# Kernel optimization log

Measured on AMD Instinct MI355X. Metric: run time of the kernel, lower is better.

## Reference

```python
import jax, jax.numpy as jnp
import numpy as np

N_NODES = 100000
N_EDGES = 1600000
IN_DIM = 256
HID = 64
OUT_DIM = 1
N_GRAPHS = 100


def setup_inputs() -> dict:
    key = jax.random.key(0)
    ks = jax.random.split(key, 12)
    x = jax.random.normal(ks[0], (N_NODES, IN_DIM), dtype=jnp.float32)
    edge_index = jax.random.randint(ks[1], (2, N_EDGES), 0, N_NODES, dtype=jnp.int64 if jax.config.read('jax_enable_x64') else jnp.int32)
    batch = jnp.sort(jax.random.randint(ks[2], (N_NODES,), 0, N_GRAPHS, dtype=jnp.int32))
    def lin(k, fan_in, fan_out):
        bound = 1.0 / np.sqrt(fan_in)
        kw, kb = jax.random.split(k)
        W = jax.random.uniform(kw, (fan_in, fan_out), minval=-bound, maxval=bound, dtype=jnp.float32)
        b = jax.random.uniform(kb, (fan_out,), minval=-bound, maxval=bound, dtype=jnp.float32)
        return W, b
    W1, b1 = lin(ks[3], IN_DIM, HID)
    W2, b2 = lin(ks[4], HID, HID)
    W3, b3 = lin(ks[5], HID, HID)
    Wl, bl = lin(ks[6], HID, OUT_DIM)
    return {"x": x, "edge_index": edge_index, "batch": batch,
            "W1": W1, "b1": b1, "W2": W2, "b2": b2, "W3": W3, "b3": b3,
            "Wl": Wl, "bl": bl}


def _gcn_layer(h, src, dst, norm, W, b):
    # PyG GCNConv: h' = scatter_add(norm * (h @ W)[src] -> dst) + b
    h = h @ W                                   # [N, F_out]
    msg = h[src] * norm[:, None]                # [E+N, F_out] irregular gather
    agg = jax.ops.segment_sum(msg, dst, num_segments=N_NODES)
    return agg + b


def reference(x, edge_index, batch, W1, b1, W2, b2, W3, b3, Wl, bl):
    # add self loops (static shape) as GCNConv does by default
    loops = jnp.arange(N_NODES, dtype=edge_index.dtype)
    src = jnp.concatenate([edge_index[0], loops])  # [E+N]
    dst = jnp.concatenate([edge_index[1], loops])  # [E+N]
    # symmetric normalization: deg over targets incl. self loops
    deg = jax.ops.segment_sum(jnp.ones_like(dst, dtype=x.dtype), dst, num_segments=N_NODES)
    dinv = jnp.where(deg > 0, jax.lax.rsqrt(deg), 0.0)
    norm = dinv[src] * dinv[dst]                # [E+N]

    h = jax.nn.relu(_gcn_layer(x, src, dst, norm, W1, b1))
    h = jax.nn.relu(_gcn_layer(h, src, dst, norm, W2, b2))
    h = _gcn_layer(h, src, dst, norm, W3, b3)   # last conv: no relu

    # global_add_pool over graphs; dropout is identity at inference
    pooled = jax.ops.segment_sum(h, batch, num_segments=N_GRAPHS)  # [G, HID]
    return pooled @ Wl + bl                     # [G, 1]
```

## Files before the change

kernel.cpp:

```cpp
#include <hip/hip_runtime.h>

#define N_NODES 100000
#define N_EDGES 1600000
#define IN_DIM 256
#define HID 64
#define N_GRAPHS 100
#define BSHIFT 8
#define NBUCK 391
#define CHUNK 4096
#define BCAP 5120

typedef __attribute__((ext_vector_type(8))) short short8;
typedef __attribute__((ext_vector_type(8))) unsigned short us8;
typedef __attribute__((ext_vector_type(4))) float floatx4;

__device__ __forceinline__ unsigned short f2b(float f) {
    unsigned int u = __float_as_uint(f);
    unsigned int r = (u + 0x7FFFu + ((u >> 16) & 1u)) >> 16;
    return (unsigned short)r;
}
__device__ __forceinline__ float b2f(unsigned short b) {
    return __uint_as_float(((unsigned int)b) << 16);
}


__global__ void k_prep(const float* __restrict__ W1, const float* __restrict__ W2,
                       const float* __restrict__ W3, const float* __restrict__ Wl,
                       const float* __restrict__ b3,
                       unsigned short* __restrict__ wt1, unsigned short* __restrict__ wt2,
                       float* __restrict__ w3l,
                       int* __restrict__ bcnt, float* __restrict__ partial) {
    int i = blockIdx.x * 256 + threadIdx.x;
    if (i < IN_DIM * HID) {
        int k = i >> 6, n = i & 63;
        wt1[n * IN_DIM + k] = f2b(W1[i]);
    }
    if (i < HID * HID) {
        int k = i >> 6, n = i & 63;
        wt2[n * HID + k] = f2b(W2[i]);
    }
    if (i < NBUCK) bcnt[i] = 0;
    if (i < N_GRAPHS * 256) partial[i] = 0.f;
    if (blockIdx.x == 0) {
        int t = threadIdx.x;
        if (t < HID) {
            float s = 0.f;
            for (int n = 0; n < HID; ++n) s += W3[t * HID + n] * Wl[n];
            w3l[t] = s;
        } else if (t == HID) {
            float s = 0.f;
            for (int n = 0; n < HID; ++n) s += b3[n] * Wl[n];
            w3l[HID] = s;
        }
    }
}


__global__ __launch_bounds__(256) void k_scatter(const int* __restrict__ src,
                                                 const int* __restrict__ dst,
                                                 int* __restrict__ bcnt,
                                                 int* __restrict__ ebuckF) {
    __shared__ int lc[NBUCK];
    const int b = blockIdx.x, t = threadIdx.x;
    for (int i = t; i < NBUCK; i += 256) lc[i] = 0;
    __syncthreads();
    const int base = b * CHUNK;
    int pk[16], bk[16], rk[16];
#pragma unroll
    for (int i = 0; i < 16; ++i) {
        int e = base + i * 256 + t;
        rk[i] = -1;
        if (e < N_EDGES) {
            int s = src[e], d = dst[e];
            bk[i] = d >> BSHIFT;
            pk[i] = (s << BSHIFT) | (d & 255);
            rk[i] = atomicAdd(&lc[bk[i]], 1);
        }
    }
    __syncthreads();
    for (int i = t; i < NBUCK; i += 256)
        lc[i] = lc[i] ? atomicAdd(&bcnt[i], lc[i]) : 0;
    __syncthreads();
#pragma unroll
    for (int i = 0; i < 16; ++i)
        if (rk[i] >= 0) {
            int p = lc[bk[i]] + rk[i];
            if (p < BCAP) ebuckF[bk[i] * BCAP + p] = pk[i];
        }
}


__global__ __launch_bounds__(256) void k_degfill(const int* __restrict__ bcnt,
                                                 const int* __restrict__ ebuckF,
                                                 int* __restrict__ deg,
                                                 float* __restrict__ dinv,
                                                 int* __restrict__ rowptr,
                                                 int* __restrict__ colF) {
    __shared__ int ld[256];
    __shared__ int sA[256];
    __shared__ int lf[256];
    const int b = blockIdx.x, t = threadIdx.x;
    const int cnt = min(bcnt[b], BCAP);
    const int ebase = b * BCAP;
    ld[t] = 1;
    __syncthreads();
    for (int j = t; j < cnt; j += 256) atomicAdd(&ld[ebuckF[ebase + j] & 255], 1);
    __syncthreads();
    const int node = (b << BSHIFT) + t;
    const int dg = ld[t];
    if (node < N_NODES) {
        deg[node] = dg;
        dinv[node] = rsqrtf((float)dg);
    }
    const int c = (node < N_NODES) ? dg - 1 : 0;
    sA[t] = c;
    __syncthreads();
    for (int off = 1; off < 256; off <<= 1) {
        int u = (t >= off) ? sA[t - off] : 0;
        __syncthreads();
        sA[t] += u;
        __syncthreads();
    }
    const int pos = ebase + sA[t] - c;
    if (node < N_NODES) rowptr[node] = pos;
    lf[t] = pos;
    __syncthreads();
    for (int j = t; j < cnt; j += 256) {
        int v = ebuckF[ebase + j];
        int p = atomicAdd(&lf[v & 255], 1);
        colF[p] = v >> BSHIFT;
    }
}


__global__ __launch_bounds__(256) void k_gemm1(const float* __restrict__ X,
                                               const unsigned short* __restrict__ Wt,
                                               const float* __restrict__ dinv,
                                               unsigned short* __restrict__ Tb) {
    __shared__ unsigned short Wb[64][264];
    const int t = threadIdx.x;
    const int lane = t & 63, wv = t >> 6;
    const int fl = lane & 15, quad = lane >> 4;
    const int r0 = blockIdx.x * 64;

    for (int g = t; g < 64 * 32; g += 256) {
        int n = g >> 5, kc8 = g & 31;
        *(us8*)&Wb[n][kc8 * 8] = *(const us8*)(Wt + n * IN_DIM + kc8 * 8);
    }

    const int arow = r0 + wv * 16 + fl;
    const bool valid = arow < N_NODES;
    const float* xp = X + (size_t)(valid ? arow : 0) * IN_DIM;

    floatx4 acc[4];
#pragma unroll
    for (int j = 0; j < 4; ++j) acc[j] = (floatx4){0.f, 0.f, 0.f, 0.f};

    __syncthreads();

#pragma unroll
    for (int kc = 0; kc < IN_DIM; kc += 32) {
        float4 x0 = make_float4(0.f, 0.f, 0.f, 0.f);
        float4 x1 = make_float4(0.f, 0.f, 0.f, 0.f);
        if (valid) {
            x0 = *(const float4*)(xp + kc + quad * 8);
            x1 = *(const float4*)(xp + kc + quad * 8 + 4);
        }
        short8 a;
        a[0] = (short)f2b(x0.x); a[1] = (short)f2b(x0.y);
        a[2] = (short)f2b(x0.z); a[3] = (short)f2b(x0.w);
        a[4] = (short)f2b(x1.x); a[5] = (short)f2b(x1.y);
        a[6] = (short)f2b(x1.z); a[7] = (short)f2b(x1.w);
#pragma unroll
        for (int ct = 0; ct < 4; ++ct) {
            short8 b = *(const short8*)&Wb[ct * 16 + fl][kc + quad * 8];
            acc[ct] = __builtin_amdgcn_mfma_f32_16x16x32_bf16(a, b, acc[ct], 0, 0, 0);
        }
    }

    int rbase = r0 + wv * 16 + quad * 4;
#pragma unroll
    for (int r = 0; r < 4; ++r) {
        int row = rbase + r;
        if (row < N_NODES) {
            float di = dinv[row];
#pragma unroll
            for (int ct = 0; ct < 4; ++ct)
                Tb[(size_t)row * HID + ct * 16 + fl] = f2b(di * acc[ct][r]);
        }
    }
}


__global__ __launch_bounds__(1024) void k_aggmm2(const unsigned short* __restrict__ Tb,
                                                 const int* __restrict__ rowptr,
                                                 const int* __restrict__ deg,
                                                 const float* __restrict__ dinv,
                                                 const int* __restrict__ col,
                                                 const float* __restrict__ bias,
                                                 const unsigned short* __restrict__ Wt,
                                                 unsigned short* __restrict__ Tb2) {
    __shared__ unsigned short Wb[64][72];
    __shared__ unsigned short Hs[16][72];
    const int t = threadIdx.x;
    const int lane = t & 63, wv = t >> 6;
    const int grp = lane >> 3, fl8 = lane & 7;

    for (int g = t; g < 64 * 8; g += 1024) {
        int n = g >> 3, kc8 = g & 7;
        *(us8*)&Wb[n][kc8 * 8] = *(const us8*)(Wt + n * HID + kc8 * 8);
    }

    const int node = blockIdx.x * 16 + wv;
    int e = __builtin_amdgcn_readfirstlane(rowptr[node]);
    const int end = e + __builtin_amdgcn_readfirstlane(deg[node]) - 1;
    float a0 = 0.f, a1 = 0.f, a2 = 0.f, a3 = 0.f;
    float a4 = 0.f, a5 = 0.f, a6 = 0.f, a7 = 0.f;
    for (; e + 16 <= end; e += 16) {
        int s0 = col[e + grp];
        int s1 = col[e + 8 + grp];
        us8 t0 = *(const us8*)(Tb + (size_t)s0 * HID + fl8 * 8);
        us8 t1 = *(const us8*)(Tb + (size_t)s1 * HID + fl8 * 8);
        a0 += b2f(t0[0]) + b2f(t1[0]); a1 += b2f(t0[1]) + b2f(t1[1]);
        a2 += b2f(t0[2]) + b2f(t1[2]); a3 += b2f(t0[3]) + b2f(t1[3]);
        a4 += b2f(t0[4]) + b2f(t1[4]); a5 += b2f(t0[5]) + b2f(t1[5]);
        a6 += b2f(t0[6]) + b2f(t1[6]); a7 += b2f(t0[7]) + b2f(t1[7]);
    }
    for (; e + 8 <= end; e += 8) {
        int s = col[e + grp];
        us8 tv = *(const us8*)(Tb + (size_t)s * HID + fl8 * 8);
        a0 += b2f(tv[0]); a1 += b2f(tv[1]); a2 += b2f(tv[2]); a3 += b2f(tv[3]);
        a4 += b2f(tv[4]); a5 += b2f(tv[5]); a6 += b2f(tv[6]); a7 += b2f(tv[7]);
    }
    if (e + grp < end) {
        int s = col[e + grp];
        us8 tv = *(const us8*)(Tb + (size_t)s * HID + fl8 * 8);
        a0 += b2f(tv[0]); a1 += b2f(tv[1]); a2 += b2f(tv[2]); a3 += b2f(tv[3]);
        a4 += b2f(tv[4]); a5 += b2f(tv[5]); a6 += b2f(tv[6]); a7 += b2f(tv[7]);
    }
    a0 += __shfl_xor(a0, 8);  a1 += __shfl_xor(a1, 8);
    a2 += __shfl_xor(a2, 8);  a3 += __shfl_xor(a3, 8);
    a4 += __shfl_xor(a4, 8);  a5 += __shfl_xor(a5, 8);
    a6 += __shfl_xor(a6, 8);  a7 += __shfl_xor(a7, 8);
    a0 += __shfl_xor(a0, 16); a1 += __shfl_xor(a1, 16);
    a2 += __shfl_xor(a2, 16); a3 += __shfl_xor(a3, 16);
    a4 += __shfl_xor(a4, 16); a5 += __shfl_xor(a5, 16);
    a6 += __shfl_xor(a6, 16); a7 += __shfl_xor(a7, 16);
    a0 += __shfl_xor(a0, 32); a1 += __shfl_xor(a1, 32);
    a2 += __shfl_xor(a2, 32); a3 += __shfl_xor(a3, 32);
    a4 += __shfl_xor(a4, 32); a5 += __shfl_xor(a5, 32);
    a6 += __shfl_xor(a6, 32); a7 += __shfl_xor(a7, 32);
    us8 sv = *(const us8*)(Tb + (size_t)node * HID + fl8 * 8);
    a0 += b2f(sv[0]); a1 += b2f(sv[1]); a2 += b2f(sv[2]); a3 += b2f(sv[3]);
    a4 += b2f(sv[4]); a5 += b2f(sv[5]); a6 += b2f(sv[6]); a7 += b2f(sv[7]);
    float di = dinv[node];
    float4 b0 = *(const float4*)(bias + fl8 * 8);
    float4 b1v = *(const float4*)(bias + fl8 * 8 + 4);
    a0 = fmaxf(fmaf(di, a0, b0.x), 0.f);
    a1 = fmaxf(fmaf(di, a1, b0.y), 0.f);
    a2 = fmaxf(fmaf(di, a2, b0.z), 0.f);
    a3 = fmaxf(fmaf(di, a3, b0.w), 0.f);
    a4 = fmaxf(fmaf(di, a4, b1v.x), 0.f);
    a5 = fmaxf(fmaf(di, a5, b1v.y), 0.f);
    a6 = fmaxf(fmaf(di, a6, b1v.z), 0.f);
    a7 = fmaxf(fmaf(di, a7, b1v.w), 0.f);
    if (grp == 0) {
        us8 o;
        o[0] = f2b(a0); o[1] = f2b(a1); o[2] = f2b(a2); o[3] = f2b(a3);
        o[4] = f2b(a4); o[5] = f2b(a5); o[6] = f2b(a6); o[7] = f2b(a7);
        *(us8*)&Hs[wv][fl8 * 8] = o;
    }
    __syncthreads();

    if (wv == 0) {
        const int fl = lane & 15, quad = lane >> 4;
        floatx4 acc[4];
#pragma unroll
        for (int j = 0; j < 4; ++j) acc[j] = (floatx4){0.f, 0.f, 0.f, 0.f};
#pragma unroll
        for (int kc = 0; kc < HID; kc += 32) {
            short8 a = *(const short8*)&Hs[fl][kc + quad * 8];
#pragma unroll
            for (int ct = 0; ct < 4; ++ct) {
                short8 b = *(const short8*)&Wb[ct * 16 + fl][kc + quad * 8];
                acc[ct] = __builtin_amdgcn_mfma_f32_16x16x32_bf16(a, b, acc[ct], 0, 0, 0);
            }
        }
        int rbase = blockIdx.x * 16 + quad * 4;
#pragma unroll
        for (int r = 0; r < 4; ++r) {
            int row = rbase + r;
            float di2 = dinv[row];
#pragma unroll
            for (int ct = 0; ct < 4; ++ct)
                Tb2[(size_t)row * HID + ct * 16 + fl] = f2b(di2 * acc[ct][r]);
        }
    }
}


__global__ __launch_bounds__(1024) void k_agg_z(const unsigned short* __restrict__ Tb,
                                                const int* __restrict__ rowptr,
                                                const int* __restrict__ deg,
                                                const float* __restrict__ dinv,
                                                const int* __restrict__ col,
                                                const float* __restrict__ bias,
                                                const float* __restrict__ w3l,
                                                float* __restrict__ z) {
    int lane = threadIdx.x & 63;
    int node = blockIdx.x * 16 + (threadIdx.x >> 6);
    int grp = lane >> 3, fl = lane & 7;
    int e = __builtin_amdgcn_readfirstlane(rowptr[node]);
    int end = e + __builtin_amdgcn_readfirstlane(deg[node]) - 1;
    float a0 = 0.f, a1 = 0.f, a2 = 0.f, a3 = 0.f;
    float a4 = 0.f, a5 = 0.f, a6 = 0.f, a7 = 0.f;
    for (; e + 16 <= end; e += 16) {
        int s0 = col[e + grp];
        int s1 = col[e + 8 + grp];
        us8 t0 = *(const us8*)(Tb + (size_t)s0 * HID + fl * 8);
        us8 t1 = *(const us8*)(Tb + (size_t)s1 * HID + fl * 8);
        a0 += b2f(t0[0]) + b2f(t1[0]); a1 += b2f(t0[1]) + b2f(t1[1]);
        a2 += b2f(t0[2]) + b2f(t1[2]); a3 += b2f(t0[3]) + b2f(t1[3]);
        a4 += b2f(t0[4]) + b2f(t1[4]); a5 += b2f(t0[5]) + b2f(t1[5]);
        a6 += b2f(t0[6]) + b2f(t1[6]); a7 += b2f(t0[7]) + b2f(t1[7]);
    }
    for (; e + 8 <= end; e += 8) {
        int s = col[e + grp];
        us8 tv = *(const us8*)(Tb + (size_t)s * HID + fl * 8);
        a0 += b2f(tv[0]); a1 += b2f(tv[1]); a2 += b2f(tv[2]); a3 += b2f(tv[3]);
        a4 += b2f(tv[4]); a5 += b2f(tv[5]); a6 += b2f(tv[6]); a7 += b2f(tv[7]);
    }
    if (e + grp < end) {
        int s = col[e + grp];
        us8 tv = *(const us8*)(Tb + (size_t)s * HID + fl * 8);
        a0 += b2f(tv[0]); a1 += b2f(tv[1]); a2 += b2f(tv[2]); a3 += b2f(tv[3]);
        a4 += b2f(tv[4]); a5 += b2f(tv[5]); a6 += b2f(tv[6]); a7 += b2f(tv[7]);
    }
    a0 += __shfl_xor(a0, 8);  a1 += __shfl_xor(a1, 8);
    a2 += __shfl_xor(a2, 8);  a3 += __shfl_xor(a3, 8);
    a4 += __shfl_xor(a4, 8);  a5 += __shfl_xor(a5, 8);
    a6 += __shfl_xor(a6, 8);  a7 += __shfl_xor(a7, 8);
    a0 += __shfl_xor(a0, 16); a1 += __shfl_xor(a1, 16);
    a2 += __shfl_xor(a2, 16); a3 += __shfl_xor(a3, 16);
    a4 += __shfl_xor(a4, 16); a5 += __shfl_xor(a5, 16);
    a6 += __shfl_xor(a6, 16); a7 += __shfl_xor(a7, 16);
    a0 += __shfl_xor(a0, 32); a1 += __shfl_xor(a1, 32);
    a2 += __shfl_xor(a2, 32); a3 += __shfl_xor(a3, 32);
    a4 += __shfl_xor(a4, 32); a5 += __shfl_xor(a5, 32);
    a6 += __shfl_xor(a6, 32); a7 += __shfl_xor(a7, 32);
    us8 sv = *(const us8*)(Tb + (size_t)node * HID + fl * 8);
    a0 += b2f(sv[0]); a1 += b2f(sv[1]); a2 += b2f(sv[2]); a3 += b2f(sv[3]);
    a4 += b2f(sv[4]); a5 += b2f(sv[5]); a6 += b2f(sv[6]); a7 += b2f(sv[7]);
    float di = dinv[node];
    float4 b0 = *(const float4*)(bias + fl * 8);
    float4 b1v = *(const float4*)(bias + fl * 8 + 4);
    a0 = fmaxf(fmaf(di, a0, b0.x), 0.f);
    a1 = fmaxf(fmaf(di, a1, b0.y), 0.f);
    a2 = fmaxf(fmaf(di, a2, b0.z), 0.f);
    a3 = fmaxf(fmaf(di, a3, b0.w), 0.f);
    a4 = fmaxf(fmaf(di, a4, b1v.x), 0.f);
    a5 = fmaxf(fmaf(di, a5, b1v.y), 0.f);
    a6 = fmaxf(fmaf(di, a6, b1v.z), 0.f);
    a7 = fmaxf(fmaf(di, a7, b1v.w), 0.f);
    float4 w0 = *(const float4*)(w3l + fl * 8);
    float4 w1v = *(const float4*)(w3l + fl * 8 + 4);
    float s = a0 * w0.x + a1 * w0.y + a2 * w0.z + a3 * w0.w +
              a4 * w1v.x + a5 * w1v.y + a6 * w1v.z + a7 * w1v.w;
    s += __shfl_xor(s, 1);
    s += __shfl_xor(s, 2);
    s += __shfl_xor(s, 4);
    if (lane == 0) z[node] = di * s;
}

__global__ __launch_bounds__(256) void k_aggpool_s(const float* __restrict__ z,
                                                   const int* __restrict__ rowptr,
                                                   const int* __restrict__ deg,
                                                   const float* __restrict__ dinv,
                                                   const int* __restrict__ col,
                                                   const float* __restrict__ w3l,
                                                   const int* __restrict__ batch,
                                                   float* __restrict__ partial) {
    int i = blockIdx.x * 256 + threadIdx.x;
    if (i >= N_NODES) return;
    int e = rowptr[i];
    int end = e + deg[i] - 1;
    float s0 = z[i], s1 = 0.f, s2 = 0.f, s3 = 0.f;
    for (; e + 4 <= end; e += 4) {
        s0 += z[col[e]];
        s1 += z[col[e + 1]];
        s2 += z[col[e + 2]];
        s3 += z[col[e + 3]];
    }
    for (; e < end; ++e) s0 += z[col[e]];
    float s = w3l[HID] + dinv[i] * (s0 + s1 + s2 + s3);
    atomicAdd(&partial[batch[i] * 256 + (blockIdx.x & 255)], s);
}

__global__ void k_pool_reduce(const float* __restrict__ partial,
                              const float* __restrict__ bl,
                              float* __restrict__ out) {
    int g = blockIdx.x, t = threadIdx.x;
    float s = partial[g * 256 + t];
    s += __shfl_xor(s, 32);
    s += __shfl_xor(s, 16);
    s += __shfl_xor(s, 8);
    s += __shfl_xor(s, 4);
    s += __shfl_xor(s, 2);
    s += __shfl_xor(s, 1);
    __shared__ float ws[4];
    if ((t & 63) == 0) ws[t >> 6] = s;
    __syncthreads();
    if (t == 0) out[g] = bl[0] + ws[0] + ws[1] + ws[2] + ws[3];
}

extern "C" void kernel_launch(void* const* d_in, const int* in_sizes, int n_in,
                              void* d_out, int out_size, void* d_ws, size_t ws_size,
                              hipStream_t stream) {
    const float* x     = (const float*)d_in[0];
    const int*   ei    = (const int*)d_in[1];
    const int*   batch = (const int*)d_in[2];
    const float* W1    = (const float*)d_in[3];
    const float* b1    = (const float*)d_in[4];
    const float* W2    = (const float*)d_in[5];
    const float* b2    = (const float*)d_in[6];
    const float* W3    = (const float*)d_in[7];
    const float* b3    = (const float*)d_in[8];
    const float* Wl    = (const float*)d_in[9];
    const float* bl    = (const float*)d_in[10];
    float* out = (float*)d_out;

    char* p = (char*)d_ws;
    unsigned short* tb = (unsigned short*)p; p += (size_t)N_NODES * HID * 2;
    unsigned short* hB = (unsigned short*)p; p += (size_t)N_NODES * HID * 2;
    int*   colF    = (int*)p;   p += (size_t)NBUCK * BCAP * 4;
    int*   ebuckF  = (int*)p;   p += (size_t)NBUCK * BCAP * 4;
    int*   deg     = (int*)p;   p += (size_t)N_NODES * 4;
    float* dinv    = (float*)p; p += (size_t)N_NODES * 4;
    int*   rowptr  = (int*)p;   p += (size_t)N_NODES * 4;
    float* z       = (float*)p; p += (size_t)N_NODES * 4;
    int*   bcnt    = (int*)p;   p += (NBUCK + 1) * 4;
    float* partial = (float*)p; p += (size_t)N_GRAPHS * 256 * 4;
    unsigned short* wt1 = (unsigned short*)p; p += (size_t)IN_DIM * HID * 2;
    unsigned short* wt2 = (unsigned short*)p; p += (size_t)HID * HID * 2;
    float* w3l     = (float*)p; p += 128 * 4;

    const int* src  = ei;
    const int* dstp = ei + N_EDGES;

    const int nb = (N_NODES + 255) / 256;
    const int cb = (N_EDGES + CHUNK - 1) / CHUNK;
    const int gemm_blocks = (N_NODES + 63) / 64;
    const int agg_blocks = N_NODES / 16;

    k_prep<<<128, 256, 0, stream>>>(W1, W2, W3, Wl, b3, wt1, wt2, w3l, bcnt, partial);
    k_scatter<<<cb, 256, 0, stream>>>(src, dstp, bcnt, ebuckF);
    k_degfill<<<NBUCK, 256, 0, stream>>>(bcnt, ebuckF, deg, dinv, rowptr, colF);

    k_gemm1<<<gemm_blocks, 256, 0, stream>>>(x, wt1, dinv, tb);
    k_aggmm2<<<agg_blocks, 1024, 0, stream>>>(tb, rowptr, deg, dinv, colF, b1, wt2, hB);
    k_agg_z<<<agg_blocks, 1024, 0, stream>>>(hB, rowptr, deg, dinv, colF, b2, w3l, z);

    k_aggpool_s<<<nb, 256, 0, stream>>>(z, rowptr, deg, dinv, colF, w3l, batch, partial);
    k_pool_reduce<<<N_GRAPHS, 256, 0, stream>>>(partial, bl, out);
}
```

Measured before the change: 363.1 us.

## Merge degree/CSR fill with first GEMM and move source dinv scaling into aggregation

The degree/CSR-fill kernel and the first dense GEMM are combined into one launch: the first NBUCK blocks build deg/dinv/rowptr/colF and the remaining blocks run the X·W1 MFMA GEMM. Both stages can then run concurrently and one launch is saved. To remove the GEMM's dependence on dinv, the source-side dinv scaling moves into the first aggregation, which now loads dinv[src] per edge and uses FMAs. This adds an extra random gather per edge and keeps Tb unscaled in bf16, which slightly changes rounding.

New measurement: 353.7 us. -2.6%, faster.

```diff
diff --git a/kernel.cpp b/kernel.cpp
--- a/kernel.cpp
+++ b/kernel.cpp
@@ -90,58 +90,59 @@
 }
 
 
-__global__ __launch_bounds__(256) void k_degfill(const int* __restrict__ bcnt,
-                                                 const int* __restrict__ ebuckF,
-                                                 int* __restrict__ deg,
-                                                 float* __restrict__ dinv,
-                                                 int* __restrict__ rowptr,
-                                                 int* __restrict__ colF) {
-    __shared__ int ld[256];
-    __shared__ int sA[256];
-    __shared__ int lf[256];
-    const int b = blockIdx.x, t = threadIdx.x;
-    const int cnt = min(bcnt[b], BCAP);
-    const int ebase = b * BCAP;
-    ld[t] = 1;
-    __syncthreads();
-    for (int j = t; j < cnt; j += 256) atomicAdd(&ld[ebuckF[ebase + j] & 255], 1);
-    __syncthreads();
-    const int node = (b << BSHIFT) + t;
-    const int dg = ld[t];
-    if (node < N_NODES) {
-        deg[node] = dg;
-        dinv[node] = rsqrtf((float)dg);
-    }
-    const int c = (node < N_NODES) ? dg - 1 : 0;
-    sA[t] = c;
-    __syncthreads();
-    for (int off = 1; off < 256; off <<= 1) {
-        int u = (t >= off) ? sA[t - off] : 0;
-        __syncthreads();
-        sA[t] += u;
-        __syncthreads();
-    }
-    const int pos = ebase + sA[t] - c;
-    if (node < N_NODES) rowptr[node] = pos;
-    lf[t] = pos;
-    __syncthreads();
-    for (int j = t; j < cnt; j += 256) {
-        int v = ebuckF[ebase + j];
-        int p = atomicAdd(&lf[v & 255], 1);
-        colF[p] = v >> BSHIFT;
-    }
-}
-
-
-__global__ __launch_bounds__(256) void k_gemm1(const float* __restrict__ X,
-                                               const unsigned short* __restrict__ Wt,
-                                               const float* __restrict__ dinv,
-                                               unsigned short* __restrict__ Tb) {
+__global__ __launch_bounds__(256) void k_dgemm1(const int* __restrict__ bcnt,
+                                                const int* __restrict__ ebuckF,
+                                                int* __restrict__ deg,
+                                                float* __restrict__ dinv,
+                                                int* __restrict__ rowptr,
+                                                int* __restrict__ colF,
+                                                const float* __restrict__ X,
+                                                const unsigned short* __restrict__ Wt,
+                                                unsigned short* __restrict__ Tb) {
     __shared__ unsigned short Wb[64][264];
     const int t = threadIdx.x;
+
+    if (blockIdx.x < NBUCK) {
+        int* ld = (int*)&Wb[0][0];
+        int* sA = ld + 256;
+        int* lf = sA + 256;
+        const int b = blockIdx.x;
+        const int cnt = min(bcnt[b], BCAP);
+        const int ebase = b * BCAP;
+        ld[t] = 1;
+        __syncthreads();
+        for (int j = t; j < cnt; j += 256) atomicAdd(&ld[ebuckF[ebase + j] & 255], 1);
+        __syncthreads();
+        const int node = (b << BSHIFT) + t;
+        const int dg = ld[t];
+        if (node < N_NODES) {
+            deg[node] = dg;
+            dinv[node] = rsqrtf((float)dg);
+        }
+        const int c = (node < N_NODES) ? dg - 1 : 0;
+        sA[t] = c;
+        __syncthreads();
+        for (int off = 1; off < 256; off <<= 1) {
+            int u = (t >= off) ? sA[t - off] : 0;
+            __syncthreads();
+            sA[t] += u;
+            __syncthreads();
+        }
+        const int pos = ebase + sA[t] - c;
+        if (node < N_NODES) rowptr[node] = pos;
+        lf[t] = pos;
+        __syncthreads();
+        for (int j = t; j < cnt; j += 256) {
+            int v = ebuckF[ebase + j];
+            int p = atomicAdd(&lf[v & 255], 1);
+            colF[p] = v >> BSHIFT;
+        }
+        return;
+    }
+
     const int lane = t & 63, wv = t >> 6;
     const int fl = lane & 15, quad = lane >> 4;
-    const int r0 = blockIdx.x * 64;
+    const int r0 = (blockIdx.x - NBUCK) * 64;
 
     for (int g = t; g < 64 * 32; g += 256) {
         int n = g >> 5, kc8 = g & 31;
@@ -183,10 +184,9 @@
     for (int r = 0; r < 4; ++r) {
         int row = rbase + r;
         if (row < N_NODES) {
-            float di = dinv[row];
 #pragma unroll
             for (int ct = 0; ct < 4; ++ct)
-                Tb[(size_t)row * HID + ct * 16 + fl] = f2b(di * acc[ct][r]);
+                Tb[(size_t)row * HID + ct * 16 + fl] = f2b(acc[ct][r]);
         }
     }
 }
@@ -214,29 +214,41 @@
     const int node = blockIdx.x * 16 + wv;
     int e = __builtin_amdgcn_readfirstlane(rowptr[node]);
     const int end = e + __builtin_amdgcn_readfirstlane(deg[node]) - 1;
+    const float di = dinv[node];
     float a0 = 0.f, a1 = 0.f, a2 = 0.f, a3 = 0.f;
     float a4 = 0.f, a5 = 0.f, a6 = 0.f, a7 = 0.f;
     for (; e + 16 <= end; e += 16) {
         int s0 = col[e + grp];
         int s1 = col[e + 8 + grp];
+        float dv0 = dinv[s0], dv1 = dinv[s1];
         us8 t0 = *(const us8*)(Tb + (size_t)s0 * HID + fl8 * 8);
         us8 t1 = *(const us8*)(Tb + (size_t)s1 * HID + fl8 * 8);
-        a0 += b2f(t0[0]) + b2f(t1[0]); a1 += b2f(t0[1]) + b2f(t1[1]);
-        a2 += b2f(t0[2]) + b2f(t1[2]); a3 += b2f(t0[3]) + b2f(t1[3]);
-        a4 += b2f(t0[4]) + b2f(t1[4]); a5 += b2f(t0[5]) + b2f(t1[5]);
-        a6 += b2f(t0[6]) + b2f(t1[6]); a7 += b2f(t0[7]) + b2f(t1[7]);
+        a0 = fmaf(dv0, b2f(t0[0]), fmaf(dv1, b2f(t1[0]), a0));
+        a1 = fmaf(dv0, b2f(t0[1]), fmaf(dv1, b2f(t1[1]), a1));
+        a2 = fmaf(dv0, b2f(t0[2]), fmaf(dv1, b2f(t1[2]), a2));
+        a3 = fmaf(dv0, b2f(t0[3]), fmaf(dv1, b2f(t1[3]), a3));
+        a4 = fmaf(dv0, b2f(t0[4]), fmaf(dv1, b2f(t1[4]), a4));
+        a5 = fmaf(dv0, b2f(t0[5]), fmaf(dv1, b2f(t1[5]), a5));
+        a6 = fmaf(dv0, b2f(t0[6]), fmaf(dv1, b2f(t1[6]), a6));
+        a7 = fmaf(dv0, b2f(t0[7]), fmaf(dv1, b2f(t1[7]), a7));
     }
     for (; e + 8 <= end; e += 8) {
         int s = col[e + grp];
+        float dv = dinv[s];
         us8 tv = *(const us8*)(Tb + (size_t)s * HID + fl8 * 8);
-        a0 += b2f(tv[0]); a1 += b2f(tv[1]); a2 += b2f(tv[2]); a3 += b2f(tv[3]);
-        a4 += b2f(tv[4]); a5 += b2f(tv[5]); a6 += b2f(tv[6]); a7 += b2f(tv[7]);
+        a0 = fmaf(dv, b2f(tv[0]), a0); a1 = fmaf(dv, b2f(tv[1]), a1);
+        a2 = fmaf(dv, b2f(tv[2]), a2); a3 = fmaf(dv, b2f(tv[3]), a3);
+        a4 = fmaf(dv, b2f(tv[4]), a4); a5 = fmaf(dv, b2f(tv[5]), a5);
+        a6 = fmaf(dv, b2f(tv[6]), a6); a7 = fmaf(dv, b2f(tv[7]), a7);
     }
     if (e + grp < end) {
         int s = col[e + grp];
+        float dv = dinv[s];
         us8 tv = *(const us8*)(Tb + (size_t)s * HID + fl8 * 8);
-        a0 += b2f(tv[0]); a1 += b2f(tv[1]); a2 += b2f(tv[2]); a3 += b2f(tv[3]);
-        a4 += b2f(tv[4]); a5 += b2f(tv[5]); a6 += b2f(tv[6]); a7 += b2f(tv[7]);
+        a0 = fmaf(dv, b2f(tv[0]), a0); a1 = fmaf(dv, b2f(tv[1]), a1);
+        a2 = fmaf(dv, b2f(tv[2]), a2); a3 = fmaf(dv, b2f(tv[3]), a3);
+        a4 = fmaf(dv, b2f(tv[4]), a4); a5 = fmaf(dv, b2f(tv[5]), a5);
+        a6 = fmaf(dv, b2f(tv[6]), a6); a7 = fmaf(dv, b2f(tv[7]), a7);
     }
     a0 += __shfl_xor(a0, 8);  a1 += __shfl_xor(a1, 8);
     a2 += __shfl_xor(a2, 8);  a3 += __shfl_xor(a3, 8);
@@ -251,9 +263,10 @@
     a4 += __shfl_xor(a4, 32); a5 += __shfl_xor(a5, 32);
     a6 += __shfl_xor(a6, 32); a7 += __shfl_xor(a7, 32);
     us8 sv = *(const us8*)(Tb + (size_t)node * HID + fl8 * 8);
-    a0 += b2f(sv[0]); a1 += b2f(sv[1]); a2 += b2f(sv[2]); a3 += b2f(sv[3]);
-    a4 += b2f(sv[4]); a5 += b2f(sv[5]); a6 += b2f(sv[6]); a7 += b2f(sv[7]);
-    float di = dinv[node];
+    a0 = fmaf(di, b2f(sv[0]), a0); a1 = fmaf(di, b2f(sv[1]), a1);
+    a2 = fmaf(di, b2f(sv[2]), a2); a3 = fmaf(di, b2f(sv[3]), a3);
+    a4 = fmaf(di, b2f(sv[4]), a4); a5 = fmaf(di, b2f(sv[5]), a5);
+    a6 = fmaf(di, b2f(sv[6]), a6); a7 = fmaf(di, b2f(sv[7]), a7);
     float4 b0 = *(const float4*)(bias + fl8 * 8);
     float4 b1v = *(const float4*)(bias + fl8 * 8 + 4);
     a0 = fmaxf(fmaf(di, a0, b0.x), 0.f);
@@ -454,9 +467,9 @@
 
     k_prep<<<128, 256, 0, stream>>>(W1, W2, W3, Wl, b3, wt1, wt2, w3l, bcnt, partial);
     k_scatter<<<cb, 256, 0, stream>>>(src, dstp, bcnt, ebuckF);
-    k_degfill<<<NBUCK, 256, 0, stream>>>(bcnt, ebuckF, deg, dinv, rowptr, colF);
-
-    k_gemm1<<<gemm_blocks, 256, 0, stream>>>(x, wt1, dinv, tb);
+    k_dgemm1<<<NBUCK + gemm_blocks, 256, 0, stream>>>(bcnt, ebuckF, deg, dinv, rowptr,
+                                                      colF, x, wt1, tb);
+
     k_aggmm2<<<agg_blocks, 1024, 0, stream>>>(tb, rowptr, deg, dinv, colF, b1, wt2, hB);
     k_agg_z<<<agg_blocks, 1024, 0, stream>>>(hB, rowptr, deg, dinv, colF, b2, w3l, z);
 
```
